# Performance work log

Measured on AMD Instinct MI355X. Metric: run time of the kernel, lower is better.

Reference implementation:

```python
import jax, jax.numpy as jnp
import numpy as np


def setup_inputs() -> dict:
    key = jax.random.key(0)
    k1, k2 = jax.random.split(key)
    B, N, C = 4, 4096, 128
    points = jax.random.normal(k1, (B, N, 3), dtype=jnp.float32)
    features = jax.random.normal(k2, (B, C, N), dtype=jnp.float32)
    return {"points": points, "features": features, "npoint": 1024}


def _square_dist(a, b):
    # a: [B, N, D], b: [B, M, D] -> [B, N, M], norm=False (no division by D)
    aa = jnp.sum(a * a, axis=-1)  # [B, N]
    bb = jnp.sum(b * b, axis=-1)  # [B, M]
    ab = jnp.einsum('bnd,bmd->bnm', a, b)  # [B, N, M]
    return aa[:, :, None] + bb[:, None, :] - 2.0 * ab


def _fps_with_dist(dist, npoint):
    # dist: [B, N, N] pairwise squared distances; sequential furthest-point selection
    B, N, _ = dist.shape

    def step(carry, _):
        mind, last = carry  # mind: [B, N] min dist to selected set; last: [B] last picked idx
        d = jnp.take_along_axis(dist, last[:, None, None], axis=1)[:, 0, :]  # [B, N]
        mind = jnp.minimum(mind, d)
        nxt = jnp.argmax(mind, axis=1).astype(jnp.int32)
        return (mind, nxt), last

    init = (jnp.full((B, N), 1e10, dtype=dist.dtype), jnp.zeros((B,), jnp.int32))
    _, idxs = jax.lax.scan(step, init, None, length=npoint)  # [npoint, B]
    return idxs.T  # [B, npoint]


def reference(points, features, npoint):
    # features_for_fps = cat([points, features^T], dim=2): [B, N, 3 + C]
    f = jnp.concatenate([points, jnp.swapaxes(features, 1, 2)], axis=2)
    dist = _square_dist(f, f)  # [B, N, N]
    return _fps_with_dist(dist, npoint)
```

## Files before the change

### kernel.cpp

```cpp
#include <hip/hip_runtime.h>

#define BB 4
#define NN 4096
#define CC 128
#define DD 131
#define NPOINT 1024

__device__ __forceinline__ float fmul_(float a, float b) { return __fmul_rn(a, b); }
__device__ __forceinline__ float fadd_(float a, float b) { return __fadd_rn(a, b); }

__global__ __launch_bounds__(256) void dist_kernel(const float* __restrict__ points,
                                                   const float* __restrict__ features,
                                                   float* __restrict__ dist) {
    __shared__ float As[67][64];
    __shared__ float Bs[67][64];
    __shared__ float s_aai[64];
    __shared__ float s_aaj[64];

    const int b  = blockIdx.z;
    const int i0 = blockIdx.x * 64;
    const int j0 = blockIdx.y * 64;
    const int tid = threadIdx.x;
    const int r = tid & 63, g = tid >> 6;
    const int tx = tid & 15;
    const int ty = tid >> 4;

    for (int k = g; k < 64; k += 4) {
        float av, bv;
        if (k < 3) {
            av = points[((size_t)b * NN + i0 + r) * 3 + k];
            bv = points[((size_t)b * NN + j0 + r) * 3 + k];
        } else {
            const float* frow = features + ((size_t)b * CC + (k - 3)) * NN;
            av = frow[i0 + r];
            bv = frow[j0 + r];
        }
        As[k][r] = av;
        Bs[k][r] = bv;
    }
    __syncthreads();

    float ph[4][8];
    if (tid < 128) {
        const int rr = tid & 63;
        const float (*S)[64] = (tid < 64) ? As : Bs;
#pragma unroll
        for (int j = 0; j < 4; ++j)
#pragma unroll
            for (int l = 0; l < 8; ++l) {
                float x = S[8 * j + l][rr];
                ph[j][l] = fmul_(x, x);
            }
#pragma unroll
        for (int j = 0; j < 4; ++j)
#pragma unroll
            for (int l = 0; l < 8; ++l) {
                float x = S[32 + 8 * j + l][rr];
                ph[j][l] = fadd_(ph[j][l], fmul_(x, x));
            }
    }

    float acc[4][4];
#pragma unroll
    for (int p = 0; p < 4; ++p)
#pragma unroll
        for (int q = 0; q < 4; ++q) acc[p][q] = 0.f;

#pragma unroll 4
    for (int kk = 0; kk < 64; ++kk) {
        float4 a4 = *(const float4*)&As[kk][4 * ty];
        float4 b4 = *(const float4*)&Bs[kk][4 * tx];
        const float a[4] = {a4.x, a4.y, a4.z, a4.w};
        const float c[4] = {b4.x, b4.y, b4.z, b4.w};
#pragma unroll
        for (int p = 0; p < 4; ++p)
#pragma unroll
            for (int q = 0; q < 4; ++q)
                acc[p][q] = __builtin_fmaf(a[p], c[q], acc[p][q]);
    }
    __syncthreads();

    for (int k = g; k < 67; k += 4) {
        const float* frow = features + ((size_t)b * CC + (64 + k - 3)) * NN;
        As[k][r] = frow[i0 + r];
        Bs[k][r] = frow[j0 + r];
    }
    __syncthreads();

    if (tid < 128) {
        const int rr = tid & 63;
        const float (*S)[64] = (tid < 64) ? As : Bs;
#pragma unroll
        for (int j = 0; j < 4; ++j)
#pragma unroll
            for (int l = 0; l < 8; ++l) {
                float x = S[8 * j + l][rr];
                ph[j][l] = fadd_(ph[j][l], fmul_(x, x));
            }
#pragma unroll
        for (int j = 0; j < 4; ++j)
#pragma unroll
            for (int l = 0; l < 8; ++l) {
                float x = S[32 + 8 * j + l][rr];
                ph[j][l] = fadd_(ph[j][l], fmul_(x, x));
            }
        float v[8];
#pragma unroll
        for (int l = 0; l < 8; ++l)
            v[l] = fadd_(fadd_(fadd_(ph[0][l], ph[1][l]), ph[2][l]), ph[3][l]);
        float h4_0 = fadd_(v[0], v[4]), h4_1 = fadd_(v[1], v[5]);
        float h4_2 = fadd_(v[2], v[6]), h4_3 = fadd_(v[3], v[7]);
        float h1 = fadd_(fadd_(h4_0, h4_2), fadd_(h4_1, h4_3));
        float t0 = S[64][rr], t1 = S[65][rr], t2 = S[66][rr];
        h1 = fadd_(h1, fmul_(t0, t0));
        h1 = fadd_(h1, fmul_(t1, t1));
        h1 = fadd_(h1, fmul_(t2, t2));
        if (tid < 64) s_aai[rr] = h1; else s_aaj[rr] = h1;
    }

#pragma unroll 4
    for (int kk = 0; kk < 67; ++kk) {
        float4 a4 = *(const float4*)&As[kk][4 * ty];
        float4 b4 = *(const float4*)&Bs[kk][4 * tx];
        const float a[4] = {a4.x, a4.y, a4.z, a4.w};
        const float c[4] = {b4.x, b4.y, b4.z, b4.w};
#pragma unroll
        for (int p = 0; p < 4; ++p)
#pragma unroll
            for (int q = 0; q < 4; ++q)
                acc[p][q] = __builtin_fmaf(a[p], c[q], acc[p][q]);
    }
    __syncthreads();

#pragma unroll
    for (int p = 0; p < 4; ++p) {
        const int i = i0 + 4 * ty + p;
        const float aai = s_aai[4 * ty + p];
        float4 o;
        o.x = __builtin_fmaf(-2.0f, acc[p][0], fadd_(aai, s_aaj[4 * tx + 0]));
        o.y = __builtin_fmaf(-2.0f, acc[p][1], fadd_(aai, s_aaj[4 * tx + 1]));
        o.z = __builtin_fmaf(-2.0f, acc[p][2], fadd_(aai, s_aaj[4 * tx + 2]));
        o.w = __builtin_fmaf(-2.0f, acc[p][3], fadd_(aai, s_aaj[4 * tx + 3]));
        *(float4*)&dist[((size_t)b * NN + i) * NN + j0 + 4 * tx] = o;
    }
}

template <int CTRL>
__device__ __forceinline__ void dpp_step(float& v, int& i) {
    int ovb = __builtin_amdgcn_update_dpp(0, __float_as_int(v), CTRL, 0xF, 0xF, false);
    int oi  = __builtin_amdgcn_update_dpp(0, i,                 CTRL, 0xF, 0xF, false);
    float ov = __int_as_float(ovb);
    if (ov > v || (ov == v && oi < i)) { v = ov; i = oi; }
}

__device__ __forceinline__ unsigned long long pack_vi(float v, int idx) {
    unsigned u = __float_as_uint(v);
    u = ((int)u >= 0) ? (u | 0x80000000u) : ~u;
    if (v == 0.0f) u = 0x80000000u;
    return ((unsigned long long)u << 32) | (unsigned)(4095 - idx);
}

__device__ __forceinline__ void upd(float& bv, int& bi, float m, int idx) {
    if (m > bv) { bv = m; bi = idx; }
}

__global__ __launch_bounds__(128, 1) void fps_kernel(const float* __restrict__ dist,
                                                     int* __restrict__ out) {
    const int b = blockIdx.x;
    const int tid = threadIdx.x;
    const int lane = tid & 63;
    const int wave = tid >> 6;
    const float* Dm = dist + (size_t)b * NN * NN;

    __shared__ unsigned long long s_slot[2][2];
    __shared__ int s_hist[NPOINT];

    float4 m0 = make_float4(1e10f, 1e10f, 1e10f, 1e10f), m1 = m0, m2 = m0, m3 = m0;
    float4 m4 = m0, m5 = m0, m6 = m0, m7 = m0;
    int last = 0;

    for (int k = 0; k < NPOINT; ++k) {
        const float* row = Dm + (size_t)last * NN + 4 * tid;
        float4 d0 = *(const float4*)&row[0];
        float4 d1 = *(const float4*)&row[512];
        float4 d2 = *(const float4*)&row[1024];
        float4 d3 = *(const float4*)&row[1536];
        float4 d4 = *(const float4*)&row[2048];
        float4 d5 = *(const float4*)&row[2560];
        float4 d6 = *(const float4*)&row[3072];
        float4 d7 = *(const float4*)&row[3584];
        __builtin_amdgcn_sched_barrier(0);

        if (tid == 0) s_hist[k] = last;

        m0.x = fminf(m0.x, d0.x); m0.y = fminf(m0.y, d0.y);
        m0.z = fminf(m0.z, d0.z); m0.w = fminf(m0.w, d0.w);
        m1.x = fminf(m1.x, d1.x); m1.y = fminf(m1.y, d1.y);
        m1.z = fminf(m1.z, d1.z); m1.w = fminf(m1.w, d1.w);
        m2.x = fminf(m2.x, d2.x); m2.y = fminf(m2.y, d2.y);
        m2.z = fminf(m2.z, d2.z); m2.w = fminf(m2.w, d2.w);
        m3.x = fminf(m3.x, d3.x); m3.y = fminf(m3.y, d3.y);
        m3.z = fminf(m3.z, d3.z); m3.w = fminf(m3.w, d3.w);
        m4.x = fminf(m4.x, d4.x); m4.y = fminf(m4.y, d4.y);
        m4.z = fminf(m4.z, d4.z); m4.w = fminf(m4.w, d4.w);
        m5.x = fminf(m5.x, d5.x); m5.y = fminf(m5.y, d5.y);
        m5.z = fminf(m5.z, d5.z); m5.w = fminf(m5.w, d5.w);
        m6.x = fminf(m6.x, d6.x); m6.y = fminf(m6.y, d6.y);
        m6.z = fminf(m6.z, d6.z); m6.w = fminf(m6.w, d6.w);
        m7.x = fminf(m7.x, d7.x); m7.y = fminf(m7.y, d7.y);
        m7.z = fminf(m7.z, d7.z); m7.w = fminf(m7.w, d7.w);

        const int t4 = 4 * tid;
        float bv = m0.x; int bi = t4;
        upd(bv, bi, m0.y, t4 + 1); upd(bv, bi, m0.z, t4 + 2); upd(bv, bi, m0.w, t4 + 3);
        upd(bv, bi, m1.x, 512 + t4);  upd(bv, bi, m1.y, 512 + t4 + 1);
        upd(bv, bi, m1.z, 512 + t4 + 2); upd(bv, bi, m1.w, 512 + t4 + 3);
        upd(bv, bi, m2.x, 1024 + t4); upd(bv, bi, m2.y, 1024 + t4 + 1);
        upd(bv, bi, m2.z, 1024 + t4 + 2); upd(bv, bi, m2.w, 1024 + t4 + 3);
        upd(bv, bi, m3.x, 1536 + t4); upd(bv, bi, m3.y, 1536 + t4 + 1);
        upd(bv, bi, m3.z, 1536 + t4 + 2); upd(bv, bi, m3.w, 1536 + t4 + 3);
        upd(bv, bi, m4.x, 2048 + t4); upd(bv, bi, m4.y, 2048 + t4 + 1);
        upd(bv, bi, m4.z, 2048 + t4 + 2); upd(bv, bi, m4.w, 2048 + t4 + 3);
        upd(bv, bi, m5.x, 2560 + t4); upd(bv, bi, m5.y, 2560 + t4 + 1);
        upd(bv, bi, m5.z, 2560 + t4 + 2); upd(bv, bi, m5.w, 2560 + t4 + 3);
        upd(bv, bi, m6.x, 3072 + t4); upd(bv, bi, m6.y, 3072 + t4 + 1);
        upd(bv, bi, m6.z, 3072 + t4 + 2); upd(bv, bi, m6.w, 3072 + t4 + 3);
        upd(bv, bi, m7.x, 3584 + t4); upd(bv, bi, m7.y, 3584 + t4 + 1);
        upd(bv, bi, m7.z, 3584 + t4 + 2); upd(bv, bi, m7.w, 3584 + t4 + 3);

        dpp_step<0xB1>(bv, bi);
        dpp_step<0x4E>(bv, bi);
        dpp_step<0x141>(bv, bi);
        dpp_step<0x140>(bv, bi);
        dpp_step<0x142>(bv, bi);
        dpp_step<0x143>(bv, bi);
        float wv = __int_as_float(__builtin_amdgcn_readlane(__float_as_int(bv), 63));
        int   wi = __builtin_amdgcn_readlane(bi, 63);

        const int p = k & 1;
        if (lane == 0) s_slot[p][wave] = pack_vi(wv, wi);
        __syncthreads();

        unsigned long long s0 = s_slot[p][0], s1 = s_slot[p][1];
        unsigned long long w = (s1 > s0) ? s1 : s0;
        last = 4095 - (int)(unsigned)(w & 0xFFFFFFFFull);
    }
    __syncthreads();

#pragma unroll
    for (int c = 0; c < 8; ++c)
        out[b * NPOINT + 128 * c + tid] = s_hist[128 * c + tid];
}

extern "C" void kernel_launch(void* const* d_in, const int* in_sizes, int n_in,
                              void* d_out, int out_size, void* d_ws, size_t ws_size,
                              hipStream_t stream) {
    const float* points   = (const float*)d_in[0];
    const float* features = (const float*)d_in[1];
    int* out = (int*)d_out;

    float* dist = (float*)d_ws;

    dim3 g(NN / 64, NN / 64, BB);
    dist_kernel<<<g, 256, 0, stream>>>(points, features, dist);

    fps_kernel<<<BB, 128, 0, stream>>>(dist, out);
}
```

Measured before the change: 1.507 ms.

## Use single-wave FPS blocks with inline-asm loads and staged waitcnt

Measured after the change: 1.796 ms. +19.2%, slower.

```diff
diff --git a/kernel.cpp b/kernel.cpp
--- a/kernel.cpp
+++ b/kernel.cpp
@@ -5,6 +5,8 @@
 #define CC 128
 #define DD 131
 #define NPOINT 1024
+
+typedef float f32x4 __attribute__((ext_vector_type(4)));
 
 __device__ __forceinline__ float fmul_(float a, float b) { return __fmul_rn(a, b); }
 __device__ __forceinline__ float fadd_(float a, float b) { return __fadd_rn(a, b); }
@@ -153,103 +155,117 @@
     if (ov > v || (ov == v && oi < i)) { v = ov; i = oi; }
 }
 
-__device__ __forceinline__ unsigned long long pack_vi(float v, int idx) {
-    unsigned u = __float_as_uint(v);
-    u = ((int)u >= 0) ? (u | 0x80000000u) : ~u;
-    if (v == 0.0f) u = 0x80000000u;
-    return ((unsigned long long)u << 32) | (unsigned)(4095 - idx);
-}
-
 __device__ __forceinline__ void upd(float& bv, int& bi, float m, int idx) {
     if (m > bv) { bv = m; bi = idx; }
 }
 
-__global__ __launch_bounds__(128, 1) void fps_kernel(const float* __restrict__ dist,
-                                                     int* __restrict__ out) {
+__device__ __forceinline__ void cmb(float& bv, int& bi, float v, int i) {
+    if (v > bv || (v == bv && i < bi)) { bv = v; bi = i; }
+}
+
+#define CHUNK(c, dd, mm, BV, BI)                                               \
+    mm[0] = fminf(mm[0], dd[0]); mm[1] = fminf(mm[1], dd[1]);                  \
+    mm[2] = fminf(mm[2], dd[2]); mm[3] = fminf(mm[3], dd[3]);                  \
+    upd(BV, BI, mm[0], 256 * c + t4 + 0);                                      \
+    upd(BV, BI, mm[1], 256 * c + t4 + 1);                                      \
+    upd(BV, BI, mm[2], 256 * c + t4 + 2);                                      \
+    upd(BV, BI, mm[3], 256 * c + t4 + 3);
+
+__global__ __launch_bounds__(64, 1) void fps_kernel(const float* __restrict__ dist,
+                                                    int* __restrict__ out) {
     const int b = blockIdx.x;
     const int tid = threadIdx.x;
-    const int lane = tid & 63;
-    const int wave = tid >> 6;
     const float* Dm = dist + (size_t)b * NN * NN;
 
-    __shared__ unsigned long long s_slot[2][2];
     __shared__ int s_hist[NPOINT];
 
-    float4 m0 = make_float4(1e10f, 1e10f, 1e10f, 1e10f), m1 = m0, m2 = m0, m3 = m0;
-    float4 m4 = m0, m5 = m0, m6 = m0, m7 = m0;
+    f32x4 m0, m1, m2, m3, m4, m5, m6, m7, m8, m9, m10, m11, m12, m13, m14, m15;
+    m0 = (f32x4)(1e10f);
+    m1 = m0; m2 = m0; m3 = m0; m4 = m0; m5 = m0; m6 = m0; m7 = m0;
+    m8 = m0; m9 = m0; m10 = m0; m11 = m0; m12 = m0; m13 = m0; m14 = m0; m15 = m0;
+
     int last = 0;
+    const int t4 = 4 * tid;
+    const unsigned vb0 = 16u * tid;
+    const unsigned vb1 = vb0 + 4096u;
+    const unsigned vb2 = vb0 + 8192u;
+    const unsigned vb3 = vb0 + 12288u;
 
     for (int k = 0; k < NPOINT; ++k) {
-        const float* row = Dm + (size_t)last * NN + 4 * tid;
-        float4 d0 = *(const float4*)&row[0];
-        float4 d1 = *(const float4*)&row[512];
-        float4 d2 = *(const float4*)&row[1024];
-        float4 d3 = *(const float4*)&row[1536];
-        float4 d4 = *(const float4*)&row[2048];
-        float4 d5 = *(const float4*)&row[2560];
-        float4 d6 = *(const float4*)&row[3072];
-        float4 d7 = *(const float4*)&row[3584];
-        __builtin_amdgcn_sched_barrier(0);
+        const float* rowbase = Dm + (size_t)last * NN;
+
+        f32x4 d0, d1, d2, d3, d4, d5, d6, d7, d8, d9, d10, d11, d12, d13, d14, d15;
+        asm volatile("global_load_dwordx4 %0, %1, %2"             : "=v"(d0)  : "v"(vb0), "s"(rowbase));
+        asm volatile("global_load_dwordx4 %0, %1, %2 offset:1024" : "=v"(d1)  : "v"(vb0), "s"(rowbase));
+        asm volatile("global_load_dwordx4 %0, %1, %2 offset:2048" : "=v"(d2)  : "v"(vb0), "s"(rowbase));
+        asm volatile("global_load_dwordx4 %0, %1, %2 offset:3072" : "=v"(d3)  : "v"(vb0), "s"(rowbase));
+        asm volatile("global_load_dwordx4 %0, %1, %2"             : "=v"(d4)  : "v"(vb1), "s"(rowbase));
+        asm volatile("global_load_dwordx4 %0, %1, %2 offset:1024" : "=v"(d5)  : "v"(vb1), "s"(rowbase));
+        asm volatile("global_load_dwordx4 %0, %1, %2 offset:2048" : "=v"(d6)  : "v"(vb1), "s"(rowbase));
+        asm volatile("global_load_dwordx4 %0, %1, %2 offset:3072" : "=v"(d7)  : "v"(vb1), "s"(rowbase));
+        asm volatile("global_load_dwordx4 %0, %1, %2"             : "=v"(d8)  : "v"(vb2), "s"(rowbase));
+        asm volatile("global_load_dwordx4 %0, %1, %2 offset:1024" : "=v"(d9)  : "v"(vb2), "s"(rowbase));
+        asm volatile("global_load_dwordx4 %0, %1, %2 offset:2048" : "=v"(d10) : "v"(vb2), "s"(rowbase));
+        asm volatile("global_load_dwordx4 %0, %1, %2 offset:3072" : "=v"(d11) : "v"(vb2), "s"(rowbase));
+        asm volatile("global_load_dwordx4 %0, %1, %2"             : "=v"(d12) : "v"(vb3), "s"(rowbase));
+        asm volatile("global_load_dwordx4 %0, %1, %2 offset:1024" : "=v"(d13) : "v"(vb3), "s"(rowbase));
+        asm volatile("global_load_dwordx4 %0, %1, %2 offset:2048" : "=v"(d14) : "v"(vb3), "s"(rowbase));
+        asm volatile("global_load_dwordx4 %0, %1, %2 offset:3072" : "=v"(d15) : "v"(vb3), "s"(rowbase));
 
         if (tid == 0) s_hist[k] = last;
 
-        m0.x = fminf(m0.x, d0.x); m0.y = fminf(m0.y, d0.y);
-        m0.z = fminf(m0.z, d0.z); m0.w = fminf(m0.w, d0.w);
-        m1.x = fminf(m1.x, d1.x); m1.y = fminf(m1.y, d1.y);
-        m1.z = fminf(m1.z, d1.z); m1.w = fminf(m1.w, d1.w);
-        m2.x = fminf(m2.x, d2.x); m2.y = fminf(m2.y, d2.y);
-        m2.z = fminf(m2.z, d2.z); m2.w = fminf(m2.w, d2.w);
-        m3.x = fminf(m3.x, d3.x); m3.y = fminf(m3.y, d3.y);
-        m3.z = fminf(m3.z, d3.z); m3.w = fminf(m3.w, d3.w);
-        m4.x = fminf(m4.x, d4.x); m4.y = fminf(m4.y, d4.y);
-        m4.z = fminf(m4.z, d4.z); m4.w = fminf(m4.w, d4.w);
-        m5.x = fminf(m5.x, d5.x); m5.y = fminf(m5.y, d5.y);
-        m5.z = fminf(m5.z, d5.z); m5.w = fminf(m5.w, d5.w);
-        m6.x = fminf(m6.x, d6.x); m6.y = fminf(m6.y, d6.y);
-        m6.z = fminf(m6.z, d6.z); m6.w = fminf(m6.w, d6.w);
-        m7.x = fminf(m7.x, d7.x); m7.y = fminf(m7.y, d7.y);
-        m7.z = fminf(m7.z, d7.z); m7.w = fminf(m7.w, d7.w);
-
-        const int t4 = 4 * tid;
-        float bv = m0.x; int bi = t4;
-        upd(bv, bi, m0.y, t4 + 1); upd(bv, bi, m0.z, t4 + 2); upd(bv, bi, m0.w, t4 + 3);
-        upd(bv, bi, m1.x, 512 + t4);  upd(bv, bi, m1.y, 512 + t4 + 1);
-        upd(bv, bi, m1.z, 512 + t4 + 2); upd(bv, bi, m1.w, 512 + t4 + 3);
-        upd(bv, bi, m2.x, 1024 + t4); upd(bv, bi, m2.y, 1024 + t4 + 1);
-        upd(bv, bi, m2.z, 1024 + t4 + 2); upd(bv, bi, m2.w, 1024 + t4 + 3);
-        upd(bv, bi, m3.x, 1536 + t4); upd(bv, bi, m3.y, 1536 + t4 + 1);
-        upd(bv, bi, m3.z, 1536 + t4 + 2); upd(bv, bi, m3.w, 1536 + t4 + 3);
-        upd(bv, bi, m4.x, 2048 + t4); upd(bv, bi, m4.y, 2048 + t4 + 1);
-        upd(bv, bi, m4.z, 2048 + t4 + 2); upd(bv, bi, m4.w, 2048 + t4 + 3);
-        upd(bv, bi, m5.x, 2560 + t4); upd(bv, bi, m5.y, 2560 + t4 + 1);
-        upd(bv, bi, m5.z, 2560 + t4 + 2); upd(bv, bi, m5.w, 2560 + t4 + 3);
-        upd(bv, bi, m6.x, 3072 + t4); upd(bv, bi, m6.y, 3072 + t4 + 1);
-        upd(bv, bi, m6.z, 3072 + t4 + 2); upd(bv, bi, m6.w, 3072 + t4 + 3);
-        upd(bv, bi, m7.x, 3584 + t4); upd(bv, bi, m7.y, 3584 + t4 + 1);
-        upd(bv, bi, m7.z, 3584 + t4 + 2); upd(bv, bi, m7.w, 3584 + t4 + 3);
-
-        dpp_step<0xB1>(bv, bi);
-        dpp_step<0x4E>(bv, bi);
-        dpp_step<0x141>(bv, bi);
-        dpp_step<0x140>(bv, bi);
-        dpp_step<0x142>(bv, bi);
-        dpp_step<0x143>(bv, bi);
-        float wv = __int_as_float(__builtin_amdgcn_readlane(__float_as_int(bv), 63));
-        int   wi = __builtin_amdgcn_readlane(bi, 63);
-
-        const int p = k & 1;
-        if (lane == 0) s_slot[p][wave] = pack_vi(wv, wi);
-        __syncthreads();
-
-        unsigned long long s0 = s_slot[p][0], s1 = s_slot[p][1];
-        unsigned long long w = (s1 > s0) ? s1 : s0;
-        last = 4095 - (int)(unsigned)(w & 0xFFFFFFFFull);
-    }
-    __syncthreads();
-
-#pragma unroll
-    for (int c = 0; c < 8; ++c)
-        out[b * NPOINT + 128 * c + tid] = s_hist[128 * c + tid];
+        float bv0 = -1e30f, bv1 = -1e30f, bv2 = -1e30f, bv3 = -1e30f;
+        int   bi0 = 0, bi1 = 0, bi2 = 0, bi3 = 0;
+
+        asm volatile("s_waitcnt vmcnt(14)" ::: "memory");
+        __builtin_amdgcn_sched_barrier(0);
+        CHUNK(0, d0, m0, bv0, bi0)
+        CHUNK(1, d1, m1, bv1, bi1)
+        asm volatile("s_waitcnt vmcnt(12)" ::: "memory");
+        __builtin_amdgcn_sched_barrier(0);
+        CHUNK(2, d2, m2, bv2, bi2)
+        CHUNK(3, d3, m3, bv3, bi3)
+        asm volatile("s_waitcnt vmcnt(10)" ::: "memory");
+        __builtin_amdgcn_sched_barrier(0);
+        CHUNK(4, d4, m4, bv0, bi0)
+        CHUNK(5, d5, m5, bv1, bi1)
+        asm volatile("s_waitcnt vmcnt(8)" ::: "memory");
+        __builtin_amdgcn_sched_barrier(0);
+        CHUNK(6, d6, m6, bv2, bi2)
+        CHUNK(7, d7, m7, bv3, bi3)
+        asm volatile("s_waitcnt vmcnt(6)" ::: "memory");
+        __builtin_amdgcn_sched_barrier(0);
+        CHUNK(8, d8, m8, bv0, bi0)
+        CHUNK(9, d9, m9, bv1, bi1)
+        asm volatile("s_waitcnt vmcnt(4)" ::: "memory");
+        __builtin_amdgcn_sched_barrier(0);
+        CHUNK(10, d10, m10, bv2, bi2)
+        CHUNK(11, d11, m11, bv3, bi3)
+        asm volatile("s_waitcnt vmcnt(2)" ::: "memory");
+        __builtin_amdgcn_sched_barrier(0);
+        CHUNK(12, d12, m12, bv0, bi0)
+        CHUNK(13, d13, m13, bv1, bi1)
+        asm volatile("s_waitcnt vmcnt(0)" ::: "memory");
+        __builtin_amdgcn_sched_barrier(0);
+        CHUNK(14, d14, m14, bv2, bi2)
+        CHUNK(15, d15, m15, bv3, bi3)
+
+        cmb(bv0, bi0, bv1, bi1);
+        cmb(bv2, bi2, bv3, bi3);
+        cmb(bv0, bi0, bv2, bi2);
+
+        dpp_step<0xB1>(bv0, bi0);
+        dpp_step<0x4E>(bv0, bi0);
+        dpp_step<0x141>(bv0, bi0);
+        dpp_step<0x140>(bv0, bi0);
+        dpp_step<0x142>(bv0, bi0);
+        dpp_step<0x143>(bv0, bi0);
+        last = __builtin_amdgcn_readlane(bi0, 63);
+    }
+
+#pragma unroll
+    for (int c = 0; c < 16; ++c)
+        out[b * NPOINT + 64 * c + tid] = s_hist[64 * c + tid];
 }
 
 extern "C" void kernel_launch(void* const* d_in, const int* in_sizes, int n_in,
@@ -264,5 +280,5 @@
     dim3 g(NN / 64, NN / 64, BB);
     dist_kernel<<<g, 256, 0, stream>>>(points, features, dist);
 
-    fps_kernel<<<BB, 128, 0, stream>>>(dist, out);
-}
+    fps_kernel<<<BB, 64, 0, stream>>>(dist, out);
+}
```

## Split each batch's FPS across eight workgroups with global-memory spin synchronization

Applied to the files above, without the earlier changes.

Measured after the change: 1.966 ms. 30.5% more time.

```diff
diff --git a/kernel.cpp b/kernel.cpp
--- a/kernel.cpp
+++ b/kernel.cpp
@@ -5,6 +5,9 @@
 #define CC 128
 #define DD 131
 #define NPOINT 1024
+#define NW 8
+
+typedef float f32x4 __attribute__((ext_vector_type(4)));
 
 __device__ __forceinline__ float fmul_(float a, float b) { return __fmul_rn(a, b); }
 __device__ __forceinline__ float fadd_(float a, float b) { return __fadd_rn(a, b); }
@@ -153,80 +156,51 @@
     if (ov > v || (ov == v && oi < i)) { v = ov; i = oi; }
 }
 
-__device__ __forceinline__ unsigned long long pack_vi(float v, int idx) {
-    unsigned u = __float_as_uint(v);
-    u = ((int)u >= 0) ? (u | 0x80000000u) : ~u;
-    if (v == 0.0f) u = 0x80000000u;
-    return ((unsigned long long)u << 32) | (unsigned)(4095 - idx);
-}
-
 __device__ __forceinline__ void upd(float& bv, int& bi, float m, int idx) {
     if (m > bv) { bv = m; bi = idx; }
 }
 
-__global__ __launch_bounds__(128, 1) void fps_kernel(const float* __restrict__ dist,
-                                                     int* __restrict__ out) {
-    const int b = blockIdx.x;
-    const int tid = threadIdx.x;
-    const int lane = tid & 63;
-    const int wave = tid >> 6;
+__device__ unsigned long long g_slots[BB][2][NW];
+__device__ unsigned int g_done[BB];
+
+__global__ __launch_bounds__(64, 1) void fps_kernel(const float* __restrict__ dist,
+                                                    int* __restrict__ out) {
+    const int bid = blockIdx.x;
+    const int b = bid >> 3;
+    const int w = bid & 7;
+    const int lane = threadIdx.x;
     const float* Dm = dist + (size_t)b * NN * NN;
 
-    __shared__ unsigned long long s_slot[2][2];
     __shared__ int s_hist[NPOINT];
 
-    float4 m0 = make_float4(1e10f, 1e10f, 1e10f, 1e10f), m1 = m0, m2 = m0, m3 = m0;
-    float4 m4 = m0, m5 = m0, m6 = m0, m7 = m0;
+    f32x4 mA = (f32x4)(1e10f), mB = (f32x4)(1e10f);
     int last = 0;
 
+    const unsigned vb = 2048u * w + 16u * lane;
+    const int baseA = 512 * w + 4 * lane;
+    const int baseB = baseA + 256;
+
     for (int k = 0; k < NPOINT; ++k) {
-        const float* row = Dm + (size_t)last * NN + 4 * tid;
-        float4 d0 = *(const float4*)&row[0];
-        float4 d1 = *(const float4*)&row[512];
-        float4 d2 = *(const float4*)&row[1024];
-        float4 d3 = *(const float4*)&row[1536];
-        float4 d4 = *(const float4*)&row[2048];
-        float4 d5 = *(const float4*)&row[2560];
-        float4 d6 = *(const float4*)&row[3072];
-        float4 d7 = *(const float4*)&row[3584];
+        if (w == 0 && lane == 0) s_hist[k] = last;
+        if (k == NPOINT - 1) break;
+
+        const float* rowbase = Dm + (size_t)last * NN;
+        f32x4 dA, dB;
+        asm volatile("global_load_dwordx4 %0, %1, %2"             : "=v"(dA) : "v"(vb), "s"(rowbase));
+        asm volatile("global_load_dwordx4 %0, %1, %2 offset:1024" : "=v"(dB) : "v"(vb), "s"(rowbase));
+        asm volatile("s_waitcnt vmcnt(0)" ::: "memory");
         __builtin_amdgcn_sched_barrier(0);
 
-        if (tid == 0) s_hist[k] = last;
-
-        m0.x = fminf(m0.x, d0.x); m0.y = fminf(m0.y, d0.y);
-        m0.z = fminf(m0.z, d0.z); m0.w = fminf(m0.w, d0.w);
-        m1.x = fminf(m1.x, d1.x); m1.y = fminf(m1.y, d1.y);
-        m1.z = fminf(m1.z, d1.z); m1.w = fminf(m1.w, d1.w);
-        m2.x = fminf(m2.x, d2.x); m2.y = fminf(m2.y, d2.y);
-        m2.z = fminf(m2.z, d2.z); m2.w = fminf(m2.w, d2.w);
-        m3.x = fminf(m3.x, d3.x); m3.y = fminf(m3.y, d3.y);
-        m3.z = fminf(m3.z, d3.z); m3.w = fminf(m3.w, d3.w);
-        m4.x = fminf(m4.x, d4.x); m4.y = fminf(m4.y, d4.y);
-        m4.z = fminf(m4.z, d4.z); m4.w = fminf(m4.w, d4.w);
-        m5.x = fminf(m5.x, d5.x); m5.y = fminf(m5.y, d5.y);
-        m5.z = fminf(m5.z, d5.z); m5.w = fminf(m5.w, d5.w);
-        m6.x = fminf(m6.x, d6.x); m6.y = fminf(m6.y, d6.y);
-        m6.z = fminf(m6.z, d6.z); m6.w = fminf(m6.w, d6.w);
-        m7.x = fminf(m7.x, d7.x); m7.y = fminf(m7.y, d7.y);
-        m7.z = fminf(m7.z, d7.z); m7.w = fminf(m7.w, d7.w);
-
-        const int t4 = 4 * tid;
-        float bv = m0.x; int bi = t4;
-        upd(bv, bi, m0.y, t4 + 1); upd(bv, bi, m0.z, t4 + 2); upd(bv, bi, m0.w, t4 + 3);
-        upd(bv, bi, m1.x, 512 + t4);  upd(bv, bi, m1.y, 512 + t4 + 1);
-        upd(bv, bi, m1.z, 512 + t4 + 2); upd(bv, bi, m1.w, 512 + t4 + 3);
-        upd(bv, bi, m2.x, 1024 + t4); upd(bv, bi, m2.y, 1024 + t4 + 1);
-        upd(bv, bi, m2.z, 1024 + t4 + 2); upd(bv, bi, m2.w, 1024 + t4 + 3);
-        upd(bv, bi, m3.x, 1536 + t4); upd(bv, bi, m3.y, 1536 + t4 + 1);
-        upd(bv, bi, m3.z, 1536 + t4 + 2); upd(bv, bi, m3.w, 1536 + t4 + 3);
-        upd(bv, bi, m4.x, 2048 + t4); upd(bv, bi, m4.y, 2048 + t4 + 1);
-        upd(bv, bi, m4.z, 2048 + t4 + 2); upd(bv, bi, m4.w, 2048 + t4 + 3);
-        upd(bv, bi, m5.x, 2560 + t4); upd(bv, bi, m5.y, 2560 + t4 + 1);
-        upd(bv, bi, m5.z, 2560 + t4 + 2); upd(bv, bi, m5.w, 2560 + t4 + 3);
-        upd(bv, bi, m6.x, 3072 + t4); upd(bv, bi, m6.y, 3072 + t4 + 1);
-        upd(bv, bi, m6.z, 3072 + t4 + 2); upd(bv, bi, m6.w, 3072 + t4 + 3);
-        upd(bv, bi, m7.x, 3584 + t4); upd(bv, bi, m7.y, 3584 + t4 + 1);
-        upd(bv, bi, m7.z, 3584 + t4 + 2); upd(bv, bi, m7.w, 3584 + t4 + 3);
+        mA[0] = fminf(mA[0], dA[0]); mA[1] = fminf(mA[1], dA[1]);
+        mA[2] = fminf(mA[2], dA[2]); mA[3] = fminf(mA[3], dA[3]);
+        mB[0] = fminf(mB[0], dB[0]); mB[1] = fminf(mB[1], dB[1]);
+        mB[2] = fminf(mB[2], dB[2]); mB[3] = fminf(mB[3], dB[3]);
+
+        float bv = mA[0]; int bi = baseA;
+        upd(bv, bi, mA[1], baseA + 1); upd(bv, bi, mA[2], baseA + 2);
+        upd(bv, bi, mA[3], baseA + 3);
+        upd(bv, bi, mB[0], baseB);     upd(bv, bi, mB[1], baseB + 1);
+        upd(bv, bi, mB[2], baseB + 2); upd(bv, bi, mB[3], baseB + 3);
 
         dpp_step<0xB1>(bv, bi);
         dpp_step<0x4E>(bv, bi);
@@ -237,19 +211,64 @@
         float wv = __int_as_float(__builtin_amdgcn_readlane(__float_as_int(bv), 63));
         int   wi = __builtin_amdgcn_readlane(bi, 63);
 
+        unsigned u = __float_as_uint(wv);
+        u = ((int)u >= 0) ? (u | 0x80000000u) : ~u;
+        if (wv == 0.0f) u = 0x80000000u;
+        const unsigned long long want = (unsigned long long)(k + 1);
+        const unsigned long long mykey =
+            (want << 44) | ((unsigned long long)u << 12) | (unsigned)(4095 - wi);
+
         const int p = k & 1;
-        if (lane == 0) s_slot[p][wave] = pack_vi(wv, wi);
-        __syncthreads();
-
-        unsigned long long s0 = s_slot[p][0], s1 = s_slot[p][1];
-        unsigned long long w = (s1 > s0) ? s1 : s0;
-        last = 4095 - (int)(unsigned)(w & 0xFFFFFFFFull);
-    }
-    __syncthreads();
-
-#pragma unroll
-    for (int c = 0; c < 8; ++c)
-        out[b * NPOINT + 128 * c + tid] = s_hist[128 * c + tid];
+        if (lane == 0)
+            __hip_atomic_store(&g_slots[b][p][w], mykey,
+                               __ATOMIC_RELAXED, __HIP_MEMORY_SCOPE_AGENT);
+
+        unsigned long long key = want << 44;
+        for (;;) {
+            unsigned long long v = want << 44;
+            if (lane < NW)
+                v = __hip_atomic_load(&g_slots[b][p][lane],
+                                      __ATOMIC_RELAXED, __HIP_MEMORY_SCOPE_AGENT);
+            if (__all((int)((v >> 44) == want))) { key = v; break; }
+        }
+
+#define DPP64(CTRL)                                                                     \
+        {                                                                               \
+            int lo_ = __builtin_amdgcn_update_dpp(0, (int)(unsigned)key, CTRL, 0xF, 0xF, false); \
+            int hi_ = __builtin_amdgcn_update_dpp(0, (int)(unsigned)(key >> 32), CTRL, 0xF, 0xF, false); \
+            unsigned long long o_ = ((unsigned long long)(unsigned)hi_ << 32) | (unsigned)lo_;   \
+            if (o_ > key) key = o_;                                                     \
+        }
+        DPP64(0xB1)
+        DPP64(0x4E)
+        DPP64(0x141)
+#undef DPP64
+
+        const int lo_s = __builtin_amdgcn_readlane((int)(unsigned)key, 0);
+        last = 4095 - (lo_s & 0xFFF);
+    }
+
+    if (w == 0) {
+#pragma unroll
+        for (int c = 0; c < 16; ++c)
+            out[b * NPOINT + 64 * c + lane] = s_hist[64 * c + lane];
+    }
+
+    if (lane == 0) {
+        unsigned old = __hip_atomic_fetch_add(&g_done[b], 1u,
+                                              __ATOMIC_RELAXED, __HIP_MEMORY_SCOPE_AGENT);
+        if (old == NW - 1) {
+#pragma unroll
+            for (int i = 0; i < NW; ++i) {
+                __hip_atomic_store(&g_slots[b][0][i], 0ull,
+                                   __ATOMIC_RELAXED, __HIP_MEMORY_SCOPE_AGENT);
+                __hip_atomic_store(&g_slots[b][1][i], 0ull,
+                                   __ATOMIC_RELAXED, __HIP_MEMORY_SCOPE_AGENT);
+            }
+            __hip_atomic_store(&g_done[b], 0u,
+                               __ATOMIC_RELAXED, __HIP_MEMORY_SCOPE_AGENT);
+        }
+    }
 }
 
 extern "C" void kernel_launch(void* const* d_in, const int* in_sizes, int n_in,
@@ -264,5 +283,5 @@
     dim3 g(NN / 64, NN / 64, BB);
     dist_kernel<<<g, 256, 0, stream>>>(points, features, dist);
 
-    fps_kernel<<<BB, 128, 0, stream>>>(dist, out);
-}
+    fps_kernel<<<BB * NW, 64, 0, stream>>>(dist, out);
+}
```

## Enlarge distance GEMM tile to 128x128 with 8x8 register micro-tiles

Applied to the files above, without the earlier changes.

Result: no change. 1.526 ms (+1.3%).

```diff
diff --git a/kernel.cpp b/kernel.cpp
--- a/kernel.cpp
+++ b/kernel.cpp
@@ -12,20 +12,21 @@
 __global__ __launch_bounds__(256) void dist_kernel(const float* __restrict__ points,
                                                    const float* __restrict__ features,
                                                    float* __restrict__ dist) {
-    __shared__ float As[67][64];
-    __shared__ float Bs[67][64];
-    __shared__ float s_aai[64];
-    __shared__ float s_aaj[64];
+    __shared__ float As[67][128];
+    __shared__ float Bs[67][128];
+    __shared__ float s_aai[128];
+    __shared__ float s_aaj[128];
 
     const int b  = blockIdx.z;
-    const int i0 = blockIdx.x * 64;
-    const int j0 = blockIdx.y * 64;
+    const int i0 = blockIdx.x * 128;
+    const int j0 = blockIdx.y * 128;
     const int tid = threadIdx.x;
-    const int r = tid & 63, g = tid >> 6;
+    const int r = tid & 127, g = tid >> 7;
     const int tx = tid & 15;
-    const int ty = tid >> 4;
-
-    for (int k = g; k < 64; k += 4) {
+    const int tyy = tid >> 4;
+    const int px = ((tx & 3) << 2) | (tx >> 2);
+
+    for (int k = g; k < 64; k += 2) {
         float av, bv;
         if (k < 3) {
             av = points[((size_t)b * NN + i0 + r) * 3 + k];
@@ -41,9 +42,9 @@
     __syncthreads();
 
     float ph[4][8];
-    if (tid < 128) {
-        const int rr = tid & 63;
-        const float (*S)[64] = (tid < 64) ? As : Bs;
+    {
+        const int rr = tid & 127;
+        const float (*S)[128] = (tid < 128) ? As : Bs;
 #pragma unroll
         for (int j = 0; j < 4; ++j)
 #pragma unroll
@@ -60,36 +61,38 @@
             }
     }
 
-    float acc[4][4];
-#pragma unroll
-    for (int p = 0; p < 4; ++p)
-#pragma unroll
-        for (int q = 0; q < 4; ++q) acc[p][q] = 0.f;
-
-#pragma unroll 4
+    float acc[8][8];
+#pragma unroll
+    for (int p = 0; p < 8; ++p)
+#pragma unroll
+        for (int q = 0; q < 8; ++q) acc[p][q] = 0.f;
+
+#pragma unroll 2
     for (int kk = 0; kk < 64; ++kk) {
-        float4 a4 = *(const float4*)&As[kk][4 * ty];
-        float4 b4 = *(const float4*)&Bs[kk][4 * tx];
-        const float a[4] = {a4.x, a4.y, a4.z, a4.w};
-        const float c[4] = {b4.x, b4.y, b4.z, b4.w};
-#pragma unroll
-        for (int p = 0; p < 4; ++p)
-#pragma unroll
-            for (int q = 0; q < 4; ++q)
+        float4 a0 = *(const float4*)&As[kk][8 * tyy];
+        float4 a1 = *(const float4*)&As[kk][8 * tyy + 4];
+        float4 b0 = *(const float4*)&Bs[kk][8 * px];
+        float4 b1 = *(const float4*)&Bs[kk][8 * px + 4];
+        const float a[8] = {a0.x, a0.y, a0.z, a0.w, a1.x, a1.y, a1.z, a1.w};
+        const float c[8] = {b0.x, b0.y, b0.z, b0.w, b1.x, b1.y, b1.z, b1.w};
+#pragma unroll
+        for (int p = 0; p < 8; ++p)
+#pragma unroll
+            for (int q = 0; q < 8; ++q)
                 acc[p][q] = __builtin_fmaf(a[p], c[q], acc[p][q]);
     }
     __syncthreads();
 
-    for (int k = g; k < 67; k += 4) {
+    for (int k = g; k < 67; k += 2) {
         const float* frow = features + ((size_t)b * CC + (64 + k - 3)) * NN;
         As[k][r] = frow[i0 + r];
         Bs[k][r] = frow[j0 + r];
     }
     __syncthreads();
 
-    if (tid < 128) {
-        const int rr = tid & 63;
-        const float (*S)[64] = (tid < 64) ? As : Bs;
+    {
+        const int rr = tid & 127;
+        const float (*S)[128] = (tid < 128) ? As : Bs;
 #pragma unroll
         for (int j = 0; j < 4; ++j)
 #pragma unroll
@@ -115,33 +118,41 @@
         h1 = fadd_(h1, fmul_(t0, t0));
         h1 = fadd_(h1, fmul_(t1, t1));
         h1 = fadd_(h1, fmul_(t2, t2));
-        if (tid < 64) s_aai[rr] = h1; else s_aaj[rr] = h1;
-    }
-
-#pragma unroll 4
+        if (tid < 128) s_aai[rr] = h1; else s_aaj[rr] = h1;
+    }
+
+#pragma unroll 2
     for (int kk = 0; kk < 67; ++kk) {
-        float4 a4 = *(const float4*)&As[kk][4 * ty];
-        float4 b4 = *(const float4*)&Bs[kk][4 * tx];
-        const float a[4] = {a4.x, a4.y, a4.z, a4.w};
-        const float c[4] = {b4.x, b4.y, b4.z, b4.w};
-#pragma unroll
-        for (int p = 0; p < 4; ++p)
-#pragma unroll
-            for (int q = 0; q < 4; ++q)
+        float4 a0 = *(const float4*)&As[kk][8 * tyy];
+        float4 a1 = *(const float4*)&As[kk][8 * tyy + 4];
+        float4 b0 = *(const float4*)&Bs[kk][8 * px];
+        float4 b1 = *(const float4*)&Bs[kk][8 * px + 4];
+        const float a[8] = {a0.x, a0.y, a0.z, a0.w, a1.x, a1.y, a1.z, a1.w};
+        const float c[8] = {b0.x, b0.y, b0.z, b0.w, b1.x, b1.y, b1.z, b1.w};
+#pragma unroll
+        for (int p = 0; p < 8; ++p)
+#pragma unroll
+            for (int q = 0; q < 8; ++q)
                 acc[p][q] = __builtin_fmaf(a[p], c[q], acc[p][q]);
     }
     __syncthreads();
 
 #pragma unroll
-    for (int p = 0; p < 4; ++p) {
-        const int i = i0 + 4 * ty + p;
-        const float aai = s_aai[4 * ty + p];
-        float4 o;
-        o.x = __builtin_fmaf(-2.0f, acc[p][0], fadd_(aai, s_aaj[4 * tx + 0]));
-        o.y = __builtin_fmaf(-2.0f, acc[p][1], fadd_(aai, s_aaj[4 * tx + 1]));
-        o.z = __builtin_fmaf(-2.0f, acc[p][2], fadd_(aai, s_aaj[4 * tx + 2]));
-        o.w = __builtin_fmaf(-2.0f, acc[p][3], fadd_(aai, s_aaj[4 * tx + 3]));
-        *(float4*)&dist[((size_t)b * NN + i) * NN + j0 + 4 * tx] = o;
+    for (int p = 0; p < 8; ++p) {
+        const int i = i0 + 8 * tyy + p;
+        const float aai = s_aai[8 * tyy + p];
+        float4 o0, o1;
+        o0.x = __builtin_fmaf(-2.0f, acc[p][0], fadd_(aai, s_aaj[8 * px + 0]));
+        o0.y = __builtin_fmaf(-2.0f, acc[p][1], fadd_(aai, s_aaj[8 * px + 1]));
+        o0.z = __builtin_fmaf(-2.0f, acc[p][2], fadd_(aai, s_aaj[8 * px + 2]));
+        o0.w = __builtin_fmaf(-2.0f, acc[p][3], fadd_(aai, s_aaj[8 * px + 3]));
+        o1.x = __builtin_fmaf(-2.0f, acc[p][4], fadd_(aai, s_aaj[8 * px + 4]));
+        o1.y = __builtin_fmaf(-2.0f, acc[p][5], fadd_(aai, s_aaj[8 * px + 5]));
+        o1.z = __builtin_fmaf(-2.0f, acc[p][6], fadd_(aai, s_aaj[8 * px + 6]));
+        o1.w = __builtin_fmaf(-2.0f, acc[p][7], fadd_(aai, s_aaj[8 * px + 7]));
+        float* drow = &dist[((size_t)b * NN + i) * NN + j0 + 8 * px];
+        *(float4*)&drow[0] = o0;
+        *(float4*)&drow[4] = o1;
     }
 }
 
@@ -261,7 +272,7 @@
 
     float* dist = (float*)d_ws;
 
-    dim3 g(NN / 64, NN / 64, BB);
+    dim3 g(NN / 128, NN / 128, BB);
     dist_kernel<<<g, 256, 0, stream>>>(points, features, dist);
 
     fps_kernel<<<BB, 128, 0, stream>>>(dist, out);
```
